# Kernel tuning notes

Measured on AMD Instinct MI355X. Metric: run time of the kernel, lower is better.

Reference implementation:

```python
import jax, jax.numpy as jnp
import numpy as np
from jax import lax

IMSIZE = 64
A_SIZE = 8
C_SIZE = 10
P_SIZE = 100
VI_K = 30
GAMMA = 0.99


def setup_inputs() -> dict:
    key = jax.random.key(0)
    ks = jax.random.split(key, 8)
    B, SB = 32, 128
    S = IMSIZE * IMSIZE
    x = jax.random.normal(ks[0], (B, 2, IMSIZE, IMSIZE), jnp.float32)
    s1 = jax.random.randint(ks[1], (B, SB), 0, IMSIZE)
    s2 = jax.random.randint(ks[2], (B, SB), 0, IMSIZE)
    ds_state = jax.random.randint(ks[3], (S, A_SIZE, C_SIZE), 0, S)
    ds_prob = jax.random.randint(ks[4], (S, A_SIZE, C_SIZE), 0, P_SIZE)
    conv_w = jax.random.normal(ks[5], (1, 2, 3, 3), jnp.float32) * 0.1
    conv_b = jnp.zeros((1,), jnp.float32)
    # original init: arange(P)/max -> values in [0,1]
    pv = jnp.arange(P_SIZE, dtype=jnp.float32) / (P_SIZE - 1)
    lin_w = jax.random.normal(ks[6], (A_SIZE, A_SIZE), jnp.float32) * 0.1
    lin_b = jnp.zeros((A_SIZE,), jnp.float32)
    return dict(x=x, s1=s1, s2=s2, ds_state=ds_state, ds_prob=ds_prob,
                conv_w=conv_w, conv_b=conv_b, pv=pv, lin_w=lin_w, lin_b=lin_b)


def reference(x, s1, s2, ds_state, ds_prob, conv_w, conv_b, pv, lin_w, lin_b):
    B = x.shape[0]
    S = IMSIZE * IMSIZE
    # fr: 3x3 conv, 2->1 channels, SAME padding  -> sar [B, S, 1]
    sar = lax.conv_general_dilated(
        x, conv_w, window_strides=(1, 1), padding='SAME',
        dimension_numbers=('NCHW', 'OIHW', 'NCHW')) + conv_b[None, :, None, None]
    sar = sar.reshape(B, S, 1)
    # sad: done channel / 10 -> [B, S, 1, 1]
    sad = x[:, 1].reshape(B, S, 1, 1) / 10.0
    p = jnp.clip(pv, 0.0, 1.0)
    cf = ds_state.reshape(-1)                                # [S*A*C] successor state ids
    cp = p[ds_prob.reshape(-1)].reshape(1, S, A_SIZE, C_SIZE)  # gathered transition probs
    # torch.max over size-1 dim == squeeze
    v0 = sar[:, :, 0]                                        # [B, S]
    # hoist the per-iteration-constant weight: cp * gamma * (1 - sad)
    w = cp * GAMMA * (1.0 - sad)                             # [B, S, A, C]

    def step(carry, _):
        v, _q = carry
        vc = v[:, cf].reshape(B, S, A_SIZE, C_SIZE)          # gather successor values
        q = sar + jnp.sum(w * vc, axis=3)                    # [B, S, A]
        return (jnp.max(q, axis=2), q), None

    q_init = jnp.zeros((B, S, A_SIZE), x.dtype)
    (v, q), _ = lax.scan(step, (v0, q_init), None, length=VI_K)
    # final residual linear layer over the action dim
    qf = q.reshape(-1, A_SIZE)
    qf = qf @ lin_w.T + lin_b + qf
    q = qf.reshape(B, S, A_SIZE)
    # Q[i, j] = q[i, s1[i,j]*imsize + s2[i,j], :]  (vectorized gather)
    flat = s1 * IMSIZE + s2                                  # [B, state_bs]
    idx = jnp.broadcast_to(flat[:, :, None], flat.shape + (A_SIZE,))
    Q = jnp.take_along_axis(q, idx, axis=1)                  # [B, state_bs, A]
    return Q
```

## Files before the change

### kernel.cpp

```cpp
#include <hip/hip_runtime.h>
#include <math.h>

#define IMSIZE 64
#define S_SIZE 4096
#define A_SZ 8
#define C_SZ 10
#define B_SIZE 32
#define SB 128
#define VI_K 30
#define GAMMA 0.99f


__global__ void init_kernel(const float* __restrict__ x,
                            const float* __restrict__ conv_w,
                            const float* __restrict__ conv_b,
                            float* __restrict__ sar_ws,
                            float* __restrict__ coef_ws,
                            float* __restrict__ v0) {
    int t = blockIdx.x * blockDim.x + threadIdx.x;
    int b = t >> 12;
    int s = t & (S_SIZE - 1);
    int y = s >> 6, xx = s & 63;

    float acc = conv_b[0];
#pragma unroll
    for (int ic = 0; ic < 2; ++ic) {
        const float* xp = x + ((b * 2 + ic) << 12);
#pragma unroll
        for (int ky = 0; ky < 3; ++ky) {
            int yy = y + ky - 1;
            if (yy < 0 || yy >= IMSIZE) continue;
#pragma unroll
            for (int kx = 0; kx < 3; ++kx) {
                int xc = xx + kx - 1;
                if (xc < 0 || xc >= IMSIZE) continue;
                acc = fmaf(xp[(yy << 6) + xc], conv_w[(ic * 3 + ky) * 3 + kx], acc);
            }
        }
    }
    float x1 = x[((b * 2 + 1) << 12) + s];
    float coef = GAMMA * (1.0f - 0.1f * x1);

    int g = b >> 3, b8 = b & 7;
    int o = (((g << 12) + s) << 3) + b8;
    sar_ws[o]  = acc;
    coef_ws[o] = coef;
    v0[o]      = acc;
}

__global__ void pack_kernel(const int* __restrict__ ds_state,
                            const int* __restrict__ ds_prob,
                            const float* __restrict__ pv,
                            int2* __restrict__ pk) {
    int i = blockIdx.x * blockDim.x + threadIdx.x;
    if (i >= S_SIZE * A_SZ * C_SZ) return;
    int idx = ds_state[i];
    float p = pv[ds_prob[i]];
    p = fminf(fmaxf(p, 0.0f), 1.0f);
    int2 e;
    e.x = idx << 5;
    e.y = __float_as_int(p);
    pk[i] = e;
}

__global__ __launch_bounds__(512) void vi_kernel(const float* __restrict__ vin,
                                                 float* __restrict__ vout,
                                                 const float* __restrict__ sar_ws,
                                                 const float* __restrict__ coef_ws,
                                                 const int2* __restrict__ pk) {
    __shared__ float vld[8 * S_SIZE];
    const int g = blockIdx.x & 3;
    const int slice = blockIdx.x >> 2;
    const int tid = threadIdx.x;

    const float4* src4 = (const float4*)(vin + (g << 15));
    float4* dst4 = (float4*)vld;
#if __has_builtin(__builtin_amdgcn_global_load_lds)
#pragma unroll
    for (int r = 0; r < 16; ++r) {
        int i = tid + (r << 9);
        __builtin_amdgcn_global_load_lds(
            (const __attribute__((address_space(1))) void*)(src4 + i),
            (__attribute__((address_space(3))) void*)(dst4 + i), 16, 0, 0);
    }
#else
#pragma unroll
    for (int r = 0; r < 16; ++r) {
        int i = tid + (r << 9);
        dst4[i] = src4[i];
    }
#endif

    const int w = tid >> 3, a = tid & 7;
    const int s = (slice << 6) + w;

    int4 er[5];
    {
        const int4* rp = (const int4*)(pk + ((s << 3) + a) * C_SZ);
#pragma unroll
        for (int i = 0; i < 5; ++i) er[i] = rp[i];
    }
    float4 sar_lo, sar_hi, coef_lo, coef_hi;
    {
        const float4* sp = (const float4*)(sar_ws + (((g << 12) + s) << 3));
        const float4* cp = (const float4*)(coef_ws + (((g << 12) + s) << 3));
        sar_lo = sp[0]; sar_hi = sp[1];
        coef_lo = cp[0]; coef_hi = cp[1];
    }
    __syncthreads();

    float4 acc_lo = {0.f, 0.f, 0.f, 0.f};
    float4 acc_hi = {0.f, 0.f, 0.f, 0.f};
    const char* vbase = (const char*)vld;
#pragma unroll
    for (int i = 0; i < 5; ++i) {
        {
            int off = er[i].x;
            float p = __int_as_float(er[i].y);
            float4 lo = *(const float4*)(vbase + off);
            float4 hi = *(const float4*)(vbase + off + 16);
            acc_lo.x = fmaf(p, lo.x, acc_lo.x); acc_lo.y = fmaf(p, lo.y, acc_lo.y);
            acc_lo.z = fmaf(p, lo.z, acc_lo.z); acc_lo.w = fmaf(p, lo.w, acc_lo.w);
            acc_hi.x = fmaf(p, hi.x, acc_hi.x); acc_hi.y = fmaf(p, hi.y, acc_hi.y);
            acc_hi.z = fmaf(p, hi.z, acc_hi.z); acc_hi.w = fmaf(p, hi.w, acc_hi.w);
        }
        {
            int off = er[i].z;
            float p = __int_as_float(er[i].w);
            float4 lo = *(const float4*)(vbase + off);
            float4 hi = *(const float4*)(vbase + off + 16);
            acc_lo.x = fmaf(p, lo.x, acc_lo.x); acc_lo.y = fmaf(p, lo.y, acc_lo.y);
            acc_lo.z = fmaf(p, lo.z, acc_lo.z); acc_lo.w = fmaf(p, lo.w, acc_lo.w);
            acc_hi.x = fmaf(p, hi.x, acc_hi.x); acc_hi.y = fmaf(p, hi.y, acc_hi.y);
            acc_hi.z = fmaf(p, hi.z, acc_hi.z); acc_hi.w = fmaf(p, hi.w, acc_hi.w);
        }
    }

    float q[8];
    q[0] = fmaf(coef_lo.x, acc_lo.x, sar_lo.x);
    q[1] = fmaf(coef_lo.y, acc_lo.y, sar_lo.y);
    q[2] = fmaf(coef_lo.z, acc_lo.z, sar_lo.z);
    q[3] = fmaf(coef_lo.w, acc_lo.w, sar_lo.w);
    q[4] = fmaf(coef_hi.x, acc_hi.x, sar_hi.x);
    q[5] = fmaf(coef_hi.y, acc_hi.y, sar_hi.y);
    q[6] = fmaf(coef_hi.z, acc_hi.z, sar_hi.z);
    q[7] = fmaf(coef_hi.w, acc_hi.w, sar_hi.w);

#pragma unroll
    for (int off = 1; off < 8; off <<= 1) {
#pragma unroll
        for (int b = 0; b < 8; ++b)
            q[b] = fmaxf(q[b], __shfl_xor(q[b], off, 8));
    }
    float myv = q[0];
#pragma unroll
    for (int b = 1; b < 8; ++b)
        if (a == b) myv = q[b];
    vout[(g << 15) + (s << 3) + a] = myv;
}

__global__ void out_kernel(const float* __restrict__ v29,
                           const int* __restrict__ ds_state,
                           const int* __restrict__ ds_prob,
                           const float* __restrict__ pv,
                           const float* __restrict__ sar_ws,
                           const float* __restrict__ coef_ws,
                           const int* __restrict__ s1,
                           const int* __restrict__ s2,
                           const float* __restrict__ lin_w,
                           const float* __restrict__ lin_b,
                           float* __restrict__ out) {
    int t = blockIdx.x * blockDim.x + threadIdx.x;
    if (t >= B_SIZE * SB) return;
    int b = t >> 7;
    int s = s1[t] * IMSIZE + s2[t];
    int g = b >> 3, b8 = b & 7;
    int o = (((g << 12) + s) << 3) + b8;
    float sar = sar_ws[o];
    float coef = coef_ws[o];
    const float* vbase = v29 + (g << 15) + b8;

    float q[A_SZ];
#pragma unroll
    for (int a = 0; a < A_SZ; ++a) {
        float accq = 0.0f;
        int bb = (s * A_SZ + a) * C_SZ;
#pragma unroll
        for (int c = 0; c < C_SZ; ++c) {
            float p = pv[ds_prob[bb + c]];
            p = fminf(fmaxf(p, 0.0f), 1.0f);
            accq = fmaf(p, vbase[ds_state[bb + c] << 3], accq);
        }
        q[a] = fmaf(coef, accq, sar);
    }
#pragma unroll
    for (int i = 0; i < A_SZ; ++i) {
        float o2 = lin_b[i] + q[i];
#pragma unroll
        for (int a = 0; a < A_SZ; ++a)
            o2 = fmaf(q[a], lin_w[i * 8 + a], o2);
        out[t * 8 + i] = o2;
    }
}

extern "C" void kernel_launch(void* const* d_in, const int* in_sizes, int n_in,
                              void* d_out, int out_size, void* d_ws, size_t ws_size,
                              hipStream_t stream) {
    const float* x        = (const float*)d_in[0];
    const int*   s1       = (const int*)d_in[1];
    const int*   s2       = (const int*)d_in[2];
    const int*   ds_state = (const int*)d_in[3];
    const int*   ds_prob  = (const int*)d_in[4];
    const float* conv_w   = (const float*)d_in[5];
    const float* conv_b   = (const float*)d_in[6];
    const float* pv       = (const float*)d_in[7];
    const float* lin_w    = (const float*)d_in[8];
    const float* lin_b    = (const float*)d_in[9];
    float* out = (float*)d_out;

    const size_t VSZ = (size_t)B_SIZE * S_SIZE * 4;
    char* ws = (char*)d_ws;
    float* vA      = (float*)(ws);
    float* vB      = (float*)(ws + VSZ);
    float* sar_ws  = (float*)(ws + 2 * VSZ);
    float* coef_ws = (float*)(ws + 3 * VSZ);
    int2*  pk      = (int2*) (ws + 4 * VSZ);

    init_kernel<<<(B_SIZE * S_SIZE) / 256, 256, 0, stream>>>(
        x, conv_w, conv_b, sar_ws, coef_ws, vA);
    pack_kernel<<<(S_SIZE * A_SZ * C_SZ + 255) / 256, 256, 0, stream>>>(
        ds_state, ds_prob, pv, pk);

    float* vin = vA;
    float* vout = vB;
    for (int i = 0; i < VI_K - 1; ++i) {
        vi_kernel<<<256, 512, 0, stream>>>(vin, vout, sar_ws, coef_ws, pk);
        float* tmp = vin; vin = vout; vout = tmp;
    }

    out_kernel<<<(B_SIZE * SB + 255) / 256, 256, 0, stream>>>(
        vin, ds_state, ds_prob, pv, sar_ws, coef_ws, s1, s2, lin_w, lin_b, out);
}
```

Measured before the change: 271.8 us.

## Gather successor values from global/L2 instead of staging whole value slab in LDS

The value-iteration kernel no longer copies the full 128KB per-group value array into shared memory per block. Each thread now gathers its 10 successor vectors directly from global memory, relying on L2/cache, with all loads issued before the FMAs. Blocks shrink to 256 threads with 512 blocks, raising occupancy since no LDS is needed. The init and pack kernels are merged into a single launch. The trade-off is random global gathers in place of redundant bulk LDS loads.

```diff
diff --git a/kernel.cpp b/kernel.cpp
--- a/kernel.cpp
+++ b/kernel.cpp
@@ -11,129 +11,110 @@
 #define GAMMA 0.99f
 
 
-__global__ void init_kernel(const float* __restrict__ x,
-                            const float* __restrict__ conv_w,
-                            const float* __restrict__ conv_b,
-                            float* __restrict__ sar_ws,
-                            float* __restrict__ coef_ws,
-                            float* __restrict__ v0) {
-    int t = blockIdx.x * blockDim.x + threadIdx.x;
-    int b = t >> 12;
-    int s = t & (S_SIZE - 1);
-    int y = s >> 6, xx = s & 63;
-
-    float acc = conv_b[0];
-#pragma unroll
-    for (int ic = 0; ic < 2; ++ic) {
-        const float* xp = x + ((b * 2 + ic) << 12);
-#pragma unroll
-        for (int ky = 0; ky < 3; ++ky) {
-            int yy = y + ky - 1;
-            if (yy < 0 || yy >= IMSIZE) continue;
-#pragma unroll
-            for (int kx = 0; kx < 3; ++kx) {
-                int xc = xx + kx - 1;
-                if (xc < 0 || xc >= IMSIZE) continue;
-                acc = fmaf(xp[(yy << 6) + xc], conv_w[(ic * 3 + ky) * 3 + kx], acc);
+__global__ __launch_bounds__(256) void initpack_kernel(
+    const float* __restrict__ x,
+    const float* __restrict__ conv_w,
+    const float* __restrict__ conv_b,
+    const int* __restrict__ ds_state,
+    const int* __restrict__ ds_prob,
+    const float* __restrict__ pv,
+    float* __restrict__ sar_ws,
+    float* __restrict__ coef_ws,
+    float* __restrict__ v0,
+    int2* __restrict__ pk)
+{
+    int bid = blockIdx.x;
+    if (bid < 512) {
+        int t = bid * 256 + threadIdx.x;
+        int b = t >> 12;
+        int s = t & (S_SIZE - 1);
+        int y = s >> 6, xx = s & 63;
+
+        float acc = conv_b[0];
+#pragma unroll
+        for (int ic = 0; ic < 2; ++ic) {
+            const float* xp = x + ((b * 2 + ic) << 12);
+#pragma unroll
+            for (int ky = 0; ky < 3; ++ky) {
+                int yy = y + ky - 1;
+                if (yy < 0 || yy >= IMSIZE) continue;
+#pragma unroll
+                for (int kx = 0; kx < 3; ++kx) {
+                    int xc = xx + kx - 1;
+                    if (xc < 0 || xc >= IMSIZE) continue;
+                    acc = fmaf(xp[(yy << 6) + xc], conv_w[(ic * 3 + ky) * 3 + kx], acc);
+                }
             }
         }
-    }
-    float x1 = x[((b * 2 + 1) << 12) + s];
-    float coef = GAMMA * (1.0f - 0.1f * x1);
-
-    int g = b >> 3, b8 = b & 7;
-    int o = (((g << 12) + s) << 3) + b8;
-    sar_ws[o]  = acc;
-    coef_ws[o] = coef;
-    v0[o]      = acc;
-}
-
-__global__ void pack_kernel(const int* __restrict__ ds_state,
-                            const int* __restrict__ ds_prob,
-                            const float* __restrict__ pv,
-                            int2* __restrict__ pk) {
-    int i = blockIdx.x * blockDim.x + threadIdx.x;
-    if (i >= S_SIZE * A_SZ * C_SZ) return;
-    int idx = ds_state[i];
-    float p = pv[ds_prob[i]];
-    p = fminf(fmaxf(p, 0.0f), 1.0f);
-    int2 e;
-    e.x = idx << 5;
-    e.y = __float_as_int(p);
-    pk[i] = e;
-}
-
-__global__ __launch_bounds__(512) void vi_kernel(const float* __restrict__ vin,
-                                                 float* __restrict__ vout,
-                                                 const float* __restrict__ sar_ws,
-                                                 const float* __restrict__ coef_ws,
-                                                 const int2* __restrict__ pk) {
-    __shared__ float vld[8 * S_SIZE];
-    const int g = blockIdx.x & 3;
-    const int slice = blockIdx.x >> 2;
-    const int tid = threadIdx.x;
-
-    const float4* src4 = (const float4*)(vin + (g << 15));
-    float4* dst4 = (float4*)vld;
-#if __has_builtin(__builtin_amdgcn_global_load_lds)
-#pragma unroll
-    for (int r = 0; r < 16; ++r) {
-        int i = tid + (r << 9);
-        __builtin_amdgcn_global_load_lds(
-            (const __attribute__((address_space(1))) void*)(src4 + i),
-            (__attribute__((address_space(3))) void*)(dst4 + i), 16, 0, 0);
-    }
-#else
-#pragma unroll
-    for (int r = 0; r < 16; ++r) {
-        int i = tid + (r << 9);
-        dst4[i] = src4[i];
-    }
-#endif
-
-    const int w = tid >> 3, a = tid & 7;
-    const int s = (slice << 6) + w;
-
-    int4 er[5];
-    {
-        const int4* rp = (const int4*)(pk + ((s << 3) + a) * C_SZ);
-#pragma unroll
-        for (int i = 0; i < 5; ++i) er[i] = rp[i];
-    }
-    float4 sar_lo, sar_hi, coef_lo, coef_hi;
-    {
-        const float4* sp = (const float4*)(sar_ws + (((g << 12) + s) << 3));
-        const float4* cp = (const float4*)(coef_ws + (((g << 12) + s) << 3));
-        sar_lo = sp[0]; sar_hi = sp[1];
-        coef_lo = cp[0]; coef_hi = cp[1];
-    }
-    __syncthreads();
-
+        float x1 = x[((b * 2 + 1) << 12) + s];
+        float coef = GAMMA * (1.0f - 0.1f * x1);
+
+        int g = b >> 3, b8 = b & 7;
+        int o = (((g << 12) + s) << 3) + b8;
+        sar_ws[o]  = acc;
+        coef_ws[o] = coef;
+        v0[o]      = acc;
+    } else {
+        int i = (bid - 512) * 256 + threadIdx.x;
+        int idx = ds_state[i];
+        float p = pv[ds_prob[i]];
+        p = fminf(fmaxf(p, 0.0f), 1.0f);
+        int2 e;
+        e.x = idx << 5;
+        e.y = __float_as_int(p);
+        pk[i] = e;
+    }
+}
+
+__global__ __launch_bounds__(256) void vi_kernel(
+    const float* __restrict__ vin,
+    float* __restrict__ vout,
+    const float* __restrict__ sar_ws,
+    const float* __restrict__ coef_ws,
+    const int2* __restrict__ pk)
+{
+    int t = blockIdx.x * 256 + threadIdx.x;
+    int a = t & 7;
+    int s = (t >> 3) & (S_SIZE - 1);
+    int g = t >> 15;
+
+    const char* vbase = (const char*)(vin + (g << 15));
+
+    const int4* rp = (const int4*)(pk + ((s << 3) + a) * C_SZ);
+    int4 er0 = rp[0], er1 = rp[1], er2 = rp[2], er3 = rp[3], er4 = rp[4];
+
+    const float4* sp = (const float4*)(sar_ws + (((g << 12) + s) << 3));
+    const float4* cpt = (const float4*)(coef_ws + (((g << 12) + s) << 3));
+    float4 sar_lo = sp[0], sar_hi = sp[1];
+    float4 coef_lo = cpt[0], coef_hi = cpt[1];
+
+    int off[10] = {er0.x, er0.z, er1.x, er1.z, er2.x,
+                   er2.z, er3.x, er3.z, er4.x, er4.z};
+    float pr[10] = {__int_as_float(er0.y), __int_as_float(er0.w),
+                    __int_as_float(er1.y), __int_as_float(er1.w),
+                    __int_as_float(er2.y), __int_as_float(er2.w),
+                    __int_as_float(er3.y), __int_as_float(er3.w),
+                    __int_as_float(er4.y), __int_as_float(er4.w)};
+
+    float4 lo[10], hi[10];
+#pragma unroll
+    for (int c = 0; c < 10; ++c) {
+        lo[c] = *(const float4*)(vbase + off[c]);
+        hi[c] = *(const float4*)(vbase + off[c] + 16);
+    }
     float4 acc_lo = {0.f, 0.f, 0.f, 0.f};
     float4 acc_hi = {0.f, 0.f, 0.f, 0.f};
-    const char* vbase = (const char*)vld;
-#pragma unroll
-    for (int i = 0; i < 5; ++i) {
-        {
-            int off = er[i].x;
-            float p = __int_as_float(er[i].y);
-            float4 lo = *(const float4*)(vbase + off);
-            float4 hi = *(const float4*)(vbase + off + 16);
-            acc_lo.x = fmaf(p, lo.x, acc_lo.x); acc_lo.y = fmaf(p, lo.y, acc_lo.y);
-            acc_lo.z = fmaf(p, lo.z, acc_lo.z); acc_lo.w = fmaf(p, lo.w, acc_lo.w);
-            acc_hi.x = fmaf(p, hi.x, acc_hi.x); acc_hi.y = fmaf(p, hi.y, acc_hi.y);
-            acc_hi.z = fmaf(p, hi.z, acc_hi.z); acc_hi.w = fmaf(p, hi.w, acc_hi.w);
-        }
-        {
-            int off = er[i].z;
-            float p = __int_as_float(er[i].w);
-            float4 lo = *(const float4*)(vbase + off);
-            float4 hi = *(const float4*)(vbase + off + 16);
-            acc_lo.x = fmaf(p, lo.x, acc_lo.x); acc_lo.y = fmaf(p, lo.y, acc_lo.y);
-            acc_lo.z = fmaf(p, lo.z, acc_lo.z); acc_lo.w = fmaf(p, lo.w, acc_lo.w);
-            acc_hi.x = fmaf(p, hi.x, acc_hi.x); acc_hi.y = fmaf(p, hi.y, acc_hi.y);
-            acc_hi.z = fmaf(p, hi.z, acc_hi.z); acc_hi.w = fmaf(p, hi.w, acc_hi.w);
-        }
+#pragma unroll
+    for (int c = 0; c < 10; ++c) {
+        float p = pr[c];
+        acc_lo.x = fmaf(p, lo[c].x, acc_lo.x);
+        acc_lo.y = fmaf(p, lo[c].y, acc_lo.y);
+        acc_lo.z = fmaf(p, lo[c].z, acc_lo.z);
+        acc_lo.w = fmaf(p, lo[c].w, acc_lo.w);
+        acc_hi.x = fmaf(p, hi[c].x, acc_hi.x);
+        acc_hi.y = fmaf(p, hi[c].y, acc_hi.y);
+        acc_hi.z = fmaf(p, hi[c].z, acc_hi.z);
+        acc_hi.w = fmaf(p, hi[c].w, acc_hi.w);
     }
 
     float q[8];
@@ -147,10 +128,10 @@
     q[7] = fmaf(coef_hi.w, acc_hi.w, sar_hi.w);
 
 #pragma unroll
-    for (int off = 1; off < 8; off <<= 1) {
+    for (int offs = 1; offs < 8; offs <<= 1) {
 #pragma unroll
         for (int b = 0; b < 8; ++b)
-            q[b] = fmaxf(q[b], __shfl_xor(q[b], off, 8));
+            q[b] = fmaxf(q[b], __shfl_xor(q[b], offs, 8));
     }
     float myv = q[0];
 #pragma unroll
@@ -226,15 +207,13 @@
     float* coef_ws = (float*)(ws + 3 * VSZ);
     int2*  pk      = (int2*) (ws + 4 * VSZ);
 
-    init_kernel<<<(B_SIZE * S_SIZE) / 256, 256, 0, stream>>>(
-        x, conv_w, conv_b, sar_ws, coef_ws, vA);
-    pack_kernel<<<(S_SIZE * A_SZ * C_SZ + 255) / 256, 256, 0, stream>>>(
-        ds_state, ds_prob, pv, pk);
+    initpack_kernel<<<1792, 256, 0, stream>>>(
+        x, conv_w, conv_b, ds_state, ds_prob, pv, sar_ws, coef_ws, vA, pk);
 
     float* vin = vA;
     float* vout = vB;
     for (int i = 0; i < VI_K - 1; ++i) {
-        vi_kernel<<<256, 512, 0, stream>>>(vin, vout, sar_ws, coef_ws, pk);
+        vi_kernel<<<512, 256, 0, stream>>>(vin, vout, sar_ws, coef_ws, pk);
         float* tmp = vin; vin = vout; vout = tmp;
     }
 
```

Result: slower. 362.6 us (+33.4%).
